# Kernel optimization log

Hardware: AMD Instinct MI355X
Metric: run time of the kernel (lower is better)

The kernel has to match this reference:

```python
import jax, jax.numpy as jnp
import numpy as np

S, N, IN_F, OUT_F = 8, 200000, 128, 128

def setup_inputs() -> dict:
    key = jax.random.key(0)
    k1, k2, k3, k4 = jax.random.split(key, 4)
    support_matmul_input = jax.random.normal(k1, (S, N, IN_F), dtype=jnp.float32)
    weight = jax.random.normal(k2, (S, IN_F, OUT_F), dtype=jnp.float32)
    layer_attention = jax.random.normal(k3, (S,), dtype=jnp.float32)
    bias = jax.random.normal(k4, (OUT_F,), dtype=jnp.float32)
    return {
        "support_matmul_input": support_matmul_input,
        "weight": weight,
        "layer_attention": layer_attention,
        "bias": bias,
    }

def reference(support_matmul_input, weight, layer_attention, bias):
    # Faithful math: out[n,o] = sum_s attn[s] * (X[s] @ W[s])[n,o] + bias[o]
    # Expressed as a single fused einsum over the support dim; equivalent to
    # torch's matmul -> permute -> mul(attn) -> sum(dim=2) -> +bias.
    out = jnp.einsum("sni,sio,s->no", support_matmul_input, weight, layer_attention)
    return out + bias
```

## Files before the change

### kernel.cpp

```cpp
#include <hip/hip_runtime.h>


typedef __bf16 bf16x8 __attribute__((ext_vector_type(8)));
typedef float  f32x4  __attribute__((ext_vector_type(4)));

#define N_DIM 200000

__global__ void prep_w_kernel(const float* __restrict__ W,
                              const float* __restrict__ attn,
                              __bf16* __restrict__ Wt) {
    const int idx = blockIdx.x * 256 + threadIdx.x;
    const int o = idx >> 10;
    const int k = idx & 1023;
    const int s = k >> 7;
    const float v = attn[s] * W[(size_t)k * 128 + o];
    Wt[((size_t)(k >> 6) * 128 + o) * 64 + (k & 63)] = (__bf16)v;
}

__global__ __launch_bounds__(256, 2)
void mgc_kernel(const float* __restrict__ X,
                const __bf16* __restrict__ Wt,
                const float* __restrict__ bias,
                float* __restrict__ out) {
    const int tid  = threadIdx.x;
    const int lane = tid & 63;
    const int wave = tid >> 6;
    const int l15  = lane & 15;
    const int quad = lane >> 4;

    const long n0 = (long)blockIdx.x * 128;
    const long r0 = n0 + wave * 32;
    if (r0 >= N_DIM) return;

    f32x4 acc[2][8] = {};

    #pragma unroll 1
    for (int kb = 0; kb < 16; ++kb) {
        const int s  = kb >> 1;
        const int i0 = (kb & 1) * 64;
        const float*  Ab = X + ((size_t)s * N_DIM + (size_t)(r0 + l15)) * 128
                             + i0 + quad * 8;
        const __bf16* Bb = Wt + (size_t)kb * 8192 + (size_t)l15 * 64 + quad * 8;

        f32x4 a[2][2][2];
        #pragma unroll
        for (int i = 0; i < 2; ++i)
            #pragma unroll
            for (int kx = 0; kx < 2; ++kx) {
                const f32x4* p = (const f32x4*)(Ab + (size_t)(i * 16) * 128 + kx * 32);
                a[i][kx][0] = p[0];
                a[i][kx][1] = p[1];
            }

        bf16x8 bf[8][2];
        #pragma unroll
        for (int j = 0; j < 8; ++j)
            #pragma unroll
            for (int kx = 0; kx < 2; ++kx)
                bf[j][kx] = *(const bf16x8*)(Bb + (size_t)j * 1024 + kx * 32);

        bf16x8 abf[2][2];
        #pragma unroll
        for (int i = 0; i < 2; ++i)
            #pragma unroll
            for (int kx = 0; kx < 2; ++kx) {
                const f32x4 v0 = a[i][kx][0], v1 = a[i][kx][1];
                bf16x8 w;
                w[0] = (__bf16)v0.x; w[1] = (__bf16)v0.y;
                w[2] = (__bf16)v0.z; w[3] = (__bf16)v0.w;
                w[4] = (__bf16)v1.x; w[5] = (__bf16)v1.y;
                w[6] = (__bf16)v1.z; w[7] = (__bf16)v1.w;
                abf[i][kx] = w;
            }

        #pragma unroll
        for (int kx = 0; kx < 2; ++kx)
            #pragma unroll
            for (int i = 0; i < 2; ++i)
                #pragma unroll
                for (int j = 0; j < 8; ++j)
                    acc[i][j] = __builtin_amdgcn_mfma_f32_16x16x32_bf16(
                        abf[i][kx], bf[j][kx], acc[i][j], 0, 0, 0);
    }

    float bv[8];
    #pragma unroll
    for (int j = 0; j < 8; ++j)
        bv[j] = bias[j * 16 + l15];

    #pragma unroll
    for (int i = 0; i < 2; ++i) {
        #pragma unroll
        for (int reg = 0; reg < 4; ++reg) {
            const long r = r0 + i * 16 + quad * 4 + reg;
            float* orow = out + r * 128 + l15;
            #pragma unroll
            for (int j = 0; j < 8; ++j)
                __builtin_nontemporal_store(acc[i][j][reg] + bv[j], &orow[j * 16]);
        }
    }
}

extern "C" void kernel_launch(void* const* d_in, const int* in_sizes, int n_in,
                              void* d_out, int out_size, void* d_ws, size_t ws_size,
                              hipStream_t stream) {
    const float* X    = (const float*)d_in[0];
    const float* W    = (const float*)d_in[1];
    const float* attn = (const float*)d_in[2];
    const float* bias = (const float*)d_in[3];
    float* out = (float*)d_out;
    __bf16* Wt = (__bf16*)d_ws;

    prep_w_kernel<<<512, 256, 0, stream>>>(W, attn, Wt);
    const int nblocks = (N_DIM + 127) / 128;
    mgc_kernel<<<nblocks, 256, 0, stream>>>(X, Wt, bias, out);
}
```

Before: 1.221 ms.

## Software-pipeline X loads through per-wave LDS double buffer with coalesced row loads

Restructures the main loop into a two-stage software pipeline. The next K-tile of X is prefetched into registers while the current one is computed, then converted to bf16 and staged into a padded per-wave LDS buffer. X loads are now row-contiguous (8 lanes per row), which coalesces better than the MFMA-fragment layout, and MFMA operands come from LDS instead. Nontemporal output stores become plain stores. This adds register pressure and LDS traffic, and there is no barrier between the per-wave LDS writes and the cross-lane reads.

```diff
diff --git a/kernel.cpp b/kernel.cpp
--- a/kernel.cpp
+++ b/kernel.cpp
@@ -5,6 +5,7 @@
 typedef float  f32x4  __attribute__((ext_vector_type(4)));
 
 #define N_DIM 200000
+#define LDSS  72
 
 __global__ void prep_w_kernel(const float* __restrict__ W,
                               const float* __restrict__ attn,
@@ -22,66 +23,100 @@
                 const __bf16* __restrict__ Wt,
                 const float* __restrict__ bias,
                 float* __restrict__ out) {
+    __shared__ __bf16 As[2][4][32 * LDSS];
+
     const int tid  = threadIdx.x;
     const int lane = tid & 63;
     const int wave = tid >> 6;
     const int l15  = lane & 15;
     const int quad = lane >> 4;
+    const int arow = lane >> 3;
+    const int acol = (lane & 7) * 8;
 
     const long n0 = (long)blockIdx.x * 128;
-    const long r0 = n0 + wave * 32;
+    const long r0 = n0 + (long)wave * 32;
     if (r0 >= N_DIM) return;
 
-    f32x4 acc[2][8] = {};
+    __bf16* myA0 = &As[0][wave][0];
+    __bf16* myA1 = &As[1][wave][0];
+
+    f32x4  acc[2][8] = {};
+    f32x4  a0[8], a1[8];
+    bf16x8 bf[8][2];
+
+#define LOADA(t, ar) do {                                                      \
+    const int s_  = (t) >> 1;                                                  \
+    const int i0_ = ((t) & 1) * 64;                                            \
+    const float* base_ = X + ((size_t)s_ * N_DIM + (size_t)(r0 + arow)) * 128  \
+                           + i0_ + acol;                                       \
+    _Pragma("unroll")                                                          \
+    for (int p = 0; p < 4; ++p) {                                              \
+        const f32x4* src_ = (const f32x4*)(base_ + (size_t)(p * 8) * 128);     \
+        ar[2 * p]     = src_[0];                                               \
+        ar[2 * p + 1] = src_[1];                                               \
+    }                                                                          \
+} while (0)
+
+#define STAGEA(ar, dst) do {                                                   \
+    _Pragma("unroll")                                                          \
+    for (int p = 0; p < 4; ++p) {                                              \
+        const f32x4 v0_ = ar[2 * p], v1_ = ar[2 * p + 1];                      \
+        bf16x8 w_;                                                             \
+        w_[0] = (__bf16)v0_.x; w_[1] = (__bf16)v0_.y;                          \
+        w_[2] = (__bf16)v0_.z; w_[3] = (__bf16)v0_.w;                          \
+        w_[4] = (__bf16)v1_.x; w_[5] = (__bf16)v1_.y;                          \
+        w_[6] = (__bf16)v1_.z; w_[7] = (__bf16)v1_.w;                          \
+        *(bf16x8*)(&dst[(p * 8 + arow) * LDSS + acol]) = w_;                   \
+    }                                                                          \
+} while (0)
+
+#define LOADB(t) do {                                                          \
+    const __bf16* Bb_ = Wt + (size_t)(t) * 8192 + (size_t)l15 * 64 + quad * 8; \
+    _Pragma("unroll")                                                          \
+    for (int j = 0; j < 8; ++j) {                                              \
+        bf[j][0] = *(const bf16x8*)(Bb_ + (size_t)j * 1024);                   \
+        bf[j][1] = *(const bf16x8*)(Bb_ + (size_t)j * 1024 + 32);              \
+    }                                                                          \
+} while (0)
+
+#define COMP(srcA) do {                                                        \
+    _Pragma("unroll")                                                          \
+    for (int kx = 0; kx < 2; ++kx) {                                           \
+        bf16x8 af_[2];                                                         \
+        _Pragma("unroll")                                                      \
+        for (int i = 0; i < 2; ++i)                                            \
+            af_[i] = *(const bf16x8*)(&srcA[(i * 16 + l15) * LDSS              \
+                                            + kx * 32 + quad * 8]);            \
+        _Pragma("unroll")                                                      \
+        for (int i = 0; i < 2; ++i)                                            \
+            _Pragma("unroll")                                                  \
+            for (int j = 0; j < 8; ++j)                                        \
+                acc[i][j] = __builtin_amdgcn_mfma_f32_16x16x32_bf16(           \
+                    af_[i], bf[j][kx], acc[i][j], 0, 0, 0);                    \
+    }                                                                          \
+} while (0)
+
+    LOADA(0, a0);
+    LOADB(0);
+    LOADA(1, a1);
+    STAGEA(a0, myA0);
 
     #pragma unroll 1
-    for (int kb = 0; kb < 16; ++kb) {
-        const int s  = kb >> 1;
-        const int i0 = (kb & 1) * 64;
-        const float*  Ab = X + ((size_t)s * N_DIM + (size_t)(r0 + l15)) * 128
-                             + i0 + quad * 8;
-        const __bf16* Bb = Wt + (size_t)kb * 8192 + (size_t)l15 * 64 + quad * 8;
+    for (int t = 0; t <= 12; t += 2) {
+        LOADA(t + 2, a0);
+        COMP(myA0);
+        LOADB(t + 1);
+        STAGEA(a1, myA1);
+        LOADA(t + 3, a1);
+        COMP(myA1);
+        LOADB(t + 2);
+        STAGEA(a0, myA0);
+    }
 
-        f32x4 a[2][2][2];
-        #pragma unroll
-        for (int i = 0; i < 2; ++i)
-            #pragma unroll
-            for (int kx = 0; kx < 2; ++kx) {
-                const f32x4* p = (const f32x4*)(Ab + (size_t)(i * 16) * 128 + kx * 32);
-                a[i][kx][0] = p[0];
-                a[i][kx][1] = p[1];
-            }
-
-        bf16x8 bf[8][2];
-        #pragma unroll
-        for (int j = 0; j < 8; ++j)
-            #pragma unroll
-            for (int kx = 0; kx < 2; ++kx)
-                bf[j][kx] = *(const bf16x8*)(Bb + (size_t)j * 1024 + kx * 32);
-
-        bf16x8 abf[2][2];
-        #pragma unroll
-        for (int i = 0; i < 2; ++i)
-            #pragma unroll
-            for (int kx = 0; kx < 2; ++kx) {
-                const f32x4 v0 = a[i][kx][0], v1 = a[i][kx][1];
-                bf16x8 w;
-                w[0] = (__bf16)v0.x; w[1] = (__bf16)v0.y;
-                w[2] = (__bf16)v0.z; w[3] = (__bf16)v0.w;
-                w[4] = (__bf16)v1.x; w[5] = (__bf16)v1.y;
-                w[6] = (__bf16)v1.z; w[7] = (__bf16)v1.w;
-                abf[i][kx] = w;
-            }
-
-        #pragma unroll
-        for (int kx = 0; kx < 2; ++kx)
-            #pragma unroll
-            for (int i = 0; i < 2; ++i)
-                #pragma unroll
-                for (int j = 0; j < 8; ++j)
-                    acc[i][j] = __builtin_amdgcn_mfma_f32_16x16x32_bf16(
-                        abf[i][kx], bf[j][kx], acc[i][j], 0, 0, 0);
-    }
+    COMP(myA0);
+    LOADB(15);
+    STAGEA(a1, myA1);
+    COMP(myA1);
 
     float bv[8];
     #pragma unroll
@@ -96,9 +131,14 @@
             float* orow = out + r * 128 + l15;
             #pragma unroll
             for (int j = 0; j < 8; ++j)
-                __builtin_nontemporal_store(acc[i][j][reg] + bv[j], &orow[j * 16]);
+                orow[j * 16] = acc[i][j][reg] + bv[j];
         }
     }
+
+#undef LOADA
+#undef STAGEA
+#undef LOADB
+#undef COMP
 }
 
 extern "C" void kernel_launch(void* const* d_in, const int* in_sizes, int n_in,
```

After: 1.187 ms. 2.8% less time.
